# Optimization experiments

Hardware: AMD Instinct MI355X
Metric: run time of the kernel (lower is better)

Reference implementation:

```python
import jax, jax.numpy as jnp
import numpy as np

B = 16384        # batch size
K = 50           # neighbors per user (fixed for static shapes)
T = B * K        # total gathered neighbor items
NNEG = 20        # negative samples per positive
D = 128          # embedding dim
N_USERS = 100000
N_ITEMS = 100000
ALPHA = 1.0


def setup_inputs() -> dict:
    key = jax.random.key(0)
    k = jax.random.split(key, 9)
    I = jax.random.randint(k[0], (B,), 0, N_ITEMS)
    U = jax.random.randint(k[1], (B,), 0, N_USERS)
    I_neg = jax.random.randint(k[2], (B, NNEG), 0, N_ITEMS)
    I_U = jax.random.randint(k[3], (T,), 0, N_ITEMS)
    N_U = jnp.full((B,), K, dtype=jnp.int32)
    I_in_I_U = jax.random.randint(k[4], (B,), 0, 2).astype(jnp.int32)
    P_emb = jax.random.normal(k[5], (N_ITEMS, D), jnp.float32) * 0.02
    Q_emb = jax.random.normal(k[6], (N_ITEMS, D), jnp.float32) * 0.02
    b_u = jax.random.normal(k[7], (N_USERS,), jnp.float32) * 0.01
    b_i = jax.random.normal(k[8], (N_ITEMS,), jnp.float32) * 0.01
    return {"I": I, "U": U, "I_neg": I_neg, "I_U": I_U, "N_U": N_U,
            "I_in_I_U": I_in_I_U, "P_emb": P_emb, "Q_emb": Q_emb,
            "b_u": b_u, "b_i": b_i}


def reference(I, U, I_neg, I_U, N_U, I_in_I_U, P_emb, Q_emb, b_u, b_i):
    # P(.) / Q(.) abstracted as embedding lookups
    q = Q_emb[I]                     # [B, D]
    p = P_emb[I_U]                   # [T, D]
    p_self = P_emb[I]                # [B, D]

    # scatter-add neighbor embeddings into per-row sums
    U_idx = jnp.repeat(jnp.arange(B), N_U, total_repeat_length=T)  # [T]
    p_sum = jax.ops.segment_sum(p, U_idx, num_segments=B)          # [B, D]

    ind = I_in_I_U.astype(q.dtype)                                 # [B]
    p_ctx = p_sum - p_self * ind[:, None]                          # exclude self
    div = jnp.clip(N_U.astype(q.dtype) - ind, 1.0, None) ** ALPHA  # [B]
    p_ctx_avg = p_ctx / div[:, None]

    pq = jnp.sum(p_ctx_avg * q, axis=1)                            # [B]
    r = b_u[U] + b_i[I] + pq

    q_neg = Q_emb[I_neg.reshape(-1)].reshape(B, NNEG, D)
    pq_neg = jnp.einsum('bd,bnd->bn', p_ctx_avg, q_neg)            # [B, NNEG]
    r_neg = b_u[U][:, None] + b_i[I_neg] + pq_neg
    return (r, r_neg)
```

## Files before the change

### kernel.cpp

```cpp
#include <hip/hip_runtime.h>


constexpr int B_SZ    = 16384;
constexpr int K_NB    = 50;
constexpr int NNEG    = 20;
constexpr int D_DIM   = 128;
constexpr int N_ITEMS = 100000;

constexpr size_t TBL_ELEMS = (size_t)N_ITEMS * D_DIM;
constexpr size_t OFF_P   = 0;
constexpr size_t OFF_Q   = TBL_ELEMS;
constexpr size_t WS_NEED = 2 * TBL_ELEMS;

__device__ __forceinline__ uint32_t enc_e4m3(float x) {
    x = fminf(fmaxf(x, -448.f), 448.f);
    uint32_t b = __float_as_uint(x * 0x1p-120f);
    uint32_t s = b >> 31;
    uint32_t m = b & 0x7fffffffu;
    m = m + 0x7ffffu + ((m >> 20) & 1u);
    return (s << 7) | ((m >> 20) & 0x7fu);
}

#ifndef HW_FP8
#if defined(__has_builtin)
#if __has_builtin(__builtin_amdgcn_cvt_pk_f32_fp8)
#define HW_FP8 1
#endif
#endif
#endif
#ifndef HW_FP8
#define HW_FP8 0
#endif

typedef float f32x2_t __attribute__((ext_vector_type(2)));

__device__ __forceinline__ void dec_fp8x4(uint32_t w, float* f) {
#if HW_FP8
    f32x2_t lo = __builtin_amdgcn_cvt_pk_f32_fp8((int)w, false);
    f32x2_t hi = __builtin_amdgcn_cvt_pk_f32_fp8((int)w, true);
    f[0] = lo[0]; f[1] = lo[1]; f[2] = hi[0]; f[3] = hi[1];
#else
    #pragma unroll
    for (int j = 0; j < 4; ++j) {
        const uint32_t b = w >> (8 * j);
        const uint32_t bits = ((b & 0x80u) << 24) | ((b & 0x7fu) << 20);
        f[j] = __uint_as_float(bits) * 0x1p120f;
    }
#endif
}
__device__ __forceinline__ void dec_fp8x8(uint2 v, float* f) {
    dec_fp8x4(v.x, f);
    dec_fp8x4(v.y, f + 4);
}

__global__ __launch_bounds__(256) void cvt_tables(
    const float4* __restrict__ P4, const float4* __restrict__ Q4,
    unsigned char* __restrict__ ws, int p_thr)
{
    int i = blockIdx.x * blockDim.x + threadIdx.x;
    const float4* src; uint32_t* dst;
    if (i < p_thr) { src = P4; dst = (uint32_t*)(ws + OFF_P); }
    else           { src = Q4; dst = (uint32_t*)(ws + OFF_Q); i -= p_thr; }
    const float4 v = src[i];
    const uint32_t o = enc_e4m3(v.x * 64.f)
                     | (enc_e4m3(v.y * 64.f) << 8)
                     | (enc_e4m3(v.z * 64.f) << 16)
                     | (enc_e4m3(v.w * 64.f) << 24);
    dst[i] = o;
}

__global__ __launch_bounds__(256, 4) void fism_fwd_f8(
    const int* __restrict__ I,
    const int* __restrict__ U,
    const int* __restrict__ I_neg,
    const int* __restrict__ I_U,
    const int* __restrict__ N_U,
    const int* __restrict__ I_in_I_U,
    const unsigned char* __restrict__ ws,
    const float* __restrict__ b_u,
    const float* __restrict__ b_i,
    float* __restrict__ r,
    float* __restrict__ r_neg)
{
    const int wave = (blockIdx.x * blockDim.x + threadIdx.x) >> 6;
    if (wave >= B_SZ) return;
    const int lane = threadIdx.x & 63;
    const int t    = lane & 15;
    const int g    = lane >> 4;
    const int b    = wave;

    const unsigned char* Pb = ws + OFF_P;
    const unsigned char* Qb = ws + OFF_Q;

    int my_nbr = 0, my_neg = 0;
    if (lane < K_NB) my_nbr = I_U[b * K_NB + lane];
    if (lane < NNEG) my_neg = I_neg[b * NNEG + lane];
    const int   ii  = I[b];
    const int   uu  = U[b];
    const float ind = (float)I_in_I_U[b];
    const float nuf = (float)N_U[b];

    const float bu     = b_u[uu];
    const float bi_pos = b_i[ii];
    float my_bneg = 0.f;
    if (lane < NNEG) my_bneg = b_i[my_neg];

    const uint2 psu = *(const uint2*)(Pb + (size_t)ii * 128 + 8 * t);
    const uint2 qpu = *(const uint2*)(Qb + (size_t)ii * 128 + 8 * t);

    uint2 v[12];
    #pragma unroll
    for (int k = 0; k < 12; ++k) {
        const int item = __shfl(my_nbr, 4 * k + g, 64);
        v[k] = *(const uint2*)(Pb + (size_t)item * 128 + 8 * t);
    }
    const int item_t = __shfl(my_nbr, 48 + (g & 1), 64);
    uint2 vt = make_uint2(0u, 0u);
    if (g < 2) vt = *(const uint2*)(Pb + (size_t)item_t * 128 + 8 * t);

    uint2 qv[5];
    float bn[5];
    #pragma unroll
    for (int s = 0; s < 5; ++s) {
        const int n = 4 * s + g;
        const int item = __shfl(my_neg, n, 64);
        bn[s] = __shfl(my_bneg, n, 64);
        qv[s] = *(const uint2*)(Qb + (size_t)item * 128 + 8 * t);
    }

    float acc[8] = {0.f, 0.f, 0.f, 0.f, 0.f, 0.f, 0.f, 0.f};
    #pragma unroll
    for (int k = 0; k < 12; ++k) {
        float f[8]; dec_fp8x8(v[k], f);
        #pragma unroll
        for (int j = 0; j < 8; ++j) acc[j] += f[j];
    }
    {
        float f[8]; dec_fp8x8(vt, f);
        #pragma unroll
        for (int j = 0; j < 8; ++j) acc[j] += f[j];
    }
    #pragma unroll
    for (int j = 0; j < 8; ++j) {
        acc[j] += __shfl_xor(acc[j], 16, 64);
        acc[j] += __shfl_xor(acc[j], 32, 64);
    }

    float ps[8]; dec_fp8x8(psu, ps);
    const float inv = (1.0f / 4096.0f) / fmaxf(nuf - ind, 1.0f);
    float pctx[8];
    #pragma unroll
    for (int j = 0; j < 8; ++j) pctx[j] = (acc[j] - ps[j] * ind) * inv;

    {
        float qp[8]; dec_fp8x8(qpu, qp);
        float dot = 0.f;
        #pragma unroll
        for (int j = 0; j < 8; ++j) dot += pctx[j] * qp[j];
        #pragma unroll
        for (int m = 8; m > 0; m >>= 1)
            dot += __shfl_xor(dot, m, 64);
        if (lane == 0) r[b] = bu + bi_pos + dot;
    }

    #pragma unroll
    for (int s = 0; s < 5; ++s) {
        float q8[8]; dec_fp8x8(qv[s], q8);
        float d = 0.f;
        #pragma unroll
        for (int j = 0; j < 8; ++j) d += pctx[j] * q8[j];
        #pragma unroll
        for (int m = 8; m > 0; m >>= 1)
            d += __shfl_xor(d, m, 64);
        if (t == 0) r_neg[b * NNEG + 4 * s + g] = bu + bn[s] + d;
    }
}

__global__ __launch_bounds__(256) void fism_fwd(
    const int* __restrict__ I,
    const int* __restrict__ U,
    const int* __restrict__ I_neg,
    const int* __restrict__ I_U,
    const int* __restrict__ N_U,
    const int* __restrict__ I_in_I_U,
    const float* __restrict__ P,
    const float* __restrict__ Q,
    const float* __restrict__ b_u,
    const float* __restrict__ b_i,
    float* __restrict__ r,
    float* __restrict__ r_neg)
{
    const int wave = (blockIdx.x * blockDim.x + threadIdx.x) >> 6;
    if (wave >= B_SZ) return;
    const int lane = threadIdx.x & 63;
    const int sl   = lane & 31;
    const int half = lane >> 5;
    const int b    = wave;

    int my_nbr = 0, my_neg = 0;
    if (lane < K_NB)  my_nbr = I_U[b * K_NB + lane];
    if (lane < NNEG)  my_neg = I_neg[b * NNEG + lane];
    const int   ii   = I[b];
    const int   uu   = U[b];
    const float ind  = (float)I_in_I_U[b];
    const float nuf  = (float)N_U[b];

    const float bu     = b_u[uu];
    const float bi_pos = b_i[ii];
    float my_bneg = 0.f;
    if (lane < NNEG) my_bneg = b_i[my_neg];

    const float4 ps = ((const float4*)(P + (size_t)ii * D_DIM))[sl];
    const float4 qp = ((const float4*)(Q + (size_t)ii * D_DIM))[sl];

    float4 acc = {0.f, 0.f, 0.f, 0.f};
    #pragma unroll 5
    for (int k = 0; k < K_NB / 2; ++k) {
        const int item = __shfl(my_nbr, 2 * k + half, 64);
        const float4 v = ((const float4*)(P + (size_t)item * D_DIM))[sl];
        acc.x += v.x; acc.y += v.y; acc.z += v.z; acc.w += v.w;
    }
    acc.x += __shfl_xor(acc.x, 32, 64);
    acc.y += __shfl_xor(acc.y, 32, 64);
    acc.z += __shfl_xor(acc.z, 32, 64);
    acc.w += __shfl_xor(acc.w, 32, 64);

    const float inv = 1.0f / fmaxf(nuf - ind, 1.0f);
    float4 pctx;
    pctx.x = (acc.x - ps.x * ind) * inv;
    pctx.y = (acc.y - ps.y * ind) * inv;
    pctx.z = (acc.z - ps.z * ind) * inv;
    pctx.w = (acc.w - ps.w * ind) * inv;

    {
        float dot = pctx.x * qp.x + pctx.y * qp.y + pctx.z * qp.z + pctx.w * qp.w;
        #pragma unroll
        for (int m = 16; m > 0; m >>= 1)
            dot += __shfl_xor(dot, m, 64);
        if (lane == 0) r[b] = bu + bi_pos + dot;
    }

    #pragma unroll 5
    for (int tN = 0; tN < NNEG / 2; ++tN) {
        const int   n    = 2 * tN + half;
        const int   item = __shfl(my_neg,  n, 64);
        const float bnv  = __shfl(my_bneg, n, 64);
        const float4 qv  = ((const float4*)(Q + (size_t)item * D_DIM))[sl];
        float d = pctx.x * qv.x + pctx.y * qv.y + pctx.z * qv.z + pctx.w * qv.w;
        #pragma unroll
        for (int m = 16; m > 0; m >>= 1)
            d += __shfl_xor(d, m, 64);
        if (sl == 0) r_neg[b * NNEG + n] = bu + bnv + d;
    }
}

extern "C" void kernel_launch(void* const* d_in, const int* in_sizes, int n_in,
                              void* d_out, int out_size, void* d_ws, size_t ws_size,
                              hipStream_t stream) {
    const int*   I        = (const int*)d_in[0];
    const int*   U        = (const int*)d_in[1];
    const int*   I_neg    = (const int*)d_in[2];
    const int*   I_U      = (const int*)d_in[3];
    const int*   N_U      = (const int*)d_in[4];
    const int*   I_in_I_U = (const int*)d_in[5];
    const float* P_emb    = (const float*)d_in[6];
    const float* Q_emb    = (const float*)d_in[7];
    const float* b_u      = (const float*)d_in[8];
    const float* b_i      = (const float*)d_in[9];

    float* r     = (float*)d_out;
    float* r_neg = (float*)d_out + B_SZ;

    if (d_ws && ws_size >= WS_NEED) {
        unsigned char* ws = (unsigned char*)d_ws;

        const int p_thr = (int)(TBL_ELEMS / 4);
        const int total = 2 * p_thr;
        cvt_tables<<<total / 256, 256, 0, stream>>>(
            (const float4*)P_emb, (const float4*)Q_emb, ws, p_thr);

        fism_fwd_f8<<<B_SZ / 4, 256, 0, stream>>>(
            I, U, I_neg, I_U, N_U, I_in_I_U, ws, b_u, b_i, r, r_neg);
    } else {
        fism_fwd<<<B_SZ / 4, 256, 0, stream>>>(
            I, U, I_neg, I_U, N_U, I_in_I_U, P_emb, Q_emb, b_u, b_i, r, r_neg);
    }
}
```

Before: 162.9 us.

## Quantize P table to int4 with per-row scales and widen lane tiling

Replaces the FP8 copy of the P embedding table with a 4-bit symmetric quantization that stores one scale per row. This halves the bytes gathered for the 50 neighbour rows. The Q table stays FP8, and lanes are regrouped into 8 groups of 8 lanes, each handling 16 elements, so every wave gathers more rows per load step. The cost is much coarser precision for P (15 levels per row), which may break tolerance. Both the conversion pass and the gather kernel change structure.

```diff
diff --git a/kernel.cpp b/kernel.cpp
--- a/kernel.cpp
+++ b/kernel.cpp
@@ -8,9 +8,10 @@
 constexpr int N_ITEMS = 100000;
 
 constexpr size_t TBL_ELEMS = (size_t)N_ITEMS * D_DIM;
-constexpr size_t OFF_P   = 0;
-constexpr size_t OFF_Q   = TBL_ELEMS;
-constexpr size_t WS_NEED = 2 * TBL_ELEMS;
+constexpr size_t OFF_P4 = 0;
+constexpr size_t OFF_SC = (size_t)N_ITEMS * 64;
+constexpr size_t OFF_Q  = OFF_SC + (size_t)N_ITEMS * 4;
+constexpr size_t WS_NEED = OFF_Q + TBL_ELEMS;
 
 __device__ __forceinline__ uint32_t enc_e4m3(float x) {
     x = fminf(fmaxf(x, -448.f), 448.f);
@@ -48,28 +49,74 @@
     }
 #endif
 }
-__device__ __forceinline__ void dec_fp8x8(uint2 v, float* f) {
+__device__ __forceinline__ void dec_fp8x16(uint4 v, float* f) {
     dec_fp8x4(v.x, f);
     dec_fp8x4(v.y, f + 4);
-}
-
+    dec_fp8x4(v.z, f + 8);
+    dec_fp8x4(v.w, f + 12);
+}
+
+__device__ __forceinline__ void acc_i4x16(uint2 w, float sc, float* acc) {
+    #pragma unroll
+    for (int j = 0; j < 8; ++j) {
+        const int n0 = (int)((w.x >> (4 * j)) & 15u);
+        const int n1 = (int)((w.y >> (4 * j)) & 15u);
+        acc[j]     = fmaf((float)((n0 ^ 8) - 8), sc, acc[j]);
+        acc[8 + j] = fmaf((float)((n1 ^ 8) - 8), sc, acc[8 + j]);
+    }
+}
+__device__ __forceinline__ void dec_i4x16(uint2 w, float sc, float* f) {
+    #pragma unroll
+    for (int j = 0; j < 8; ++j) {
+        const int n0 = (int)((w.x >> (4 * j)) & 15u);
+        const int n1 = (int)((w.y >> (4 * j)) & 15u);
+        f[j]     = (float)((n0 ^ 8) - 8) * sc;
+        f[8 + j] = (float)((n1 ^ 8) - 8) * sc;
+    }
+}
+
+constexpr int CVT_PBLK = 6250;
+constexpr int CVT_QBLK = 12500;
 __global__ __launch_bounds__(256) void cvt_tables(
     const float4* __restrict__ P4, const float4* __restrict__ Q4,
-    unsigned char* __restrict__ ws, int p_thr)
+    unsigned char* __restrict__ ws)
 {
-    int i = blockIdx.x * blockDim.x + threadIdx.x;
-    const float4* src; uint32_t* dst;
-    if (i < p_thr) { src = P4; dst = (uint32_t*)(ws + OFF_P); }
-    else           { src = Q4; dst = (uint32_t*)(ws + OFF_Q); i -= p_thr; }
-    const float4 v = src[i];
-    const uint32_t o = enc_e4m3(v.x * 64.f)
-                     | (enc_e4m3(v.y * 64.f) << 8)
-                     | (enc_e4m3(v.z * 64.f) << 16)
-                     | (enc_e4m3(v.w * 64.f) << 24);
-    dst[i] = o;
-}
-
-__global__ __launch_bounds__(256, 4) void fism_fwd_f8(
+    if (blockIdx.x < CVT_PBLK) {
+        const int w    = (blockIdx.x * 256 + threadIdx.x) >> 6;
+        const int lane = threadIdx.x & 63;
+        const int c    = lane & 15;
+        const int row  = w * 4 + (lane >> 4);
+        const float4 a = P4[(size_t)row * 32 + 2 * c];
+        const float4 d = P4[(size_t)row * 32 + 2 * c + 1];
+        float f[8] = {a.x, a.y, a.z, a.w, d.x, d.y, d.z, d.w};
+        float m = 0.f;
+        #pragma unroll
+        for (int j = 0; j < 8; ++j) m = fmaxf(m, fabsf(f[j]));
+        #pragma unroll
+        for (int s = 1; s < 16; s <<= 1) m = fmaxf(m, __shfl_xor(m, s, 64));
+        const float delta = (m > 0.f) ? m * (1.f / 7.f) : 1.f;
+        const float invd  = (m > 0.f) ? 7.f / m : 0.f;
+        uint32_t o = 0;
+        #pragma unroll
+        for (int j = 0; j < 8; ++j) {
+            int q = (int)rintf(f[j] * invd);
+            q = max(-7, min(7, q));
+            o |= ((uint32_t)(q & 0xF)) << (4 * j);
+        }
+        ((uint32_t*)(ws + OFF_P4))[(size_t)row * 16 + c] = o;
+        if (c == 0) ((float*)(ws + OFF_SC))[row] = delta;
+    } else {
+        const int i = (blockIdx.x - CVT_PBLK) * 256 + threadIdx.x;
+        const float4 v = Q4[i];
+        const uint32_t o = enc_e4m3(v.x * 64.f)
+                         | (enc_e4m3(v.y * 64.f) << 8)
+                         | (enc_e4m3(v.z * 64.f) << 16)
+                         | (enc_e4m3(v.w * 64.f) << 24);
+        ((uint32_t*)(ws + OFF_Q))[i] = o;
+    }
+}
+
+__global__ __launch_bounds__(256, 4) void fism_fwd_i4(
     const int* __restrict__ I,
     const int* __restrict__ U,
     const int* __restrict__ I_neg,
@@ -85,11 +132,12 @@
     const int wave = (blockIdx.x * blockDim.x + threadIdx.x) >> 6;
     if (wave >= B_SZ) return;
     const int lane = threadIdx.x & 63;
-    const int t    = lane & 15;
-    const int g    = lane >> 4;
+    const int o    = lane & 7;
+    const int gg   = lane >> 3;
     const int b    = wave;
 
-    const unsigned char* Pb = ws + OFF_P;
+    const unsigned char* Pb = ws + OFF_P4;
+    const float*         Sc = (const float*)(ws + OFF_SC);
     const unsigned char* Qb = ws + OFF_Q;
 
     int my_nbr = 0, my_neg = 0;
@@ -105,74 +153,77 @@
     float my_bneg = 0.f;
     if (lane < NNEG) my_bneg = b_i[my_neg];
 
-    const uint2 psu = *(const uint2*)(Pb + (size_t)ii * 128 + 8 * t);
-    const uint2 qpu = *(const uint2*)(Qb + (size_t)ii * 128 + 8 * t);
-
-    uint2 v[12];
-    #pragma unroll
-    for (int k = 0; k < 12; ++k) {
-        const int item = __shfl(my_nbr, 4 * k + g, 64);
-        v[k] = *(const uint2*)(Pb + (size_t)item * 128 + 8 * t);
-    }
-    const int item_t = __shfl(my_nbr, 48 + (g & 1), 64);
+    const uint2 psu   = *(const uint2*)(Pb + (size_t)ii * 64 + 8 * o);
+    const float sc_ii = Sc[ii];
+    const uint4 qpu   = *(const uint4*)(Qb + (size_t)ii * 128 + 16 * o);
+
+    uint2 v[6]; float scv[6];
+    #pragma unroll
+    for (int k = 0; k < 6; ++k) {
+        const int item = __shfl(my_nbr, 8 * k + gg, 64);
+        v[k]   = *(const uint2*)(Pb + (size_t)item * 64 + 8 * o);
+        scv[k] = Sc[item];
+    }
+    const int item_t = __shfl(my_nbr, 48 + (gg & 1), 64);
     uint2 vt = make_uint2(0u, 0u);
-    if (g < 2) vt = *(const uint2*)(Pb + (size_t)item_t * 128 + 8 * t);
-
-    uint2 qv[5];
-    float bn[5];
-    #pragma unroll
-    for (int s = 0; s < 5; ++s) {
-        const int n = 4 * s + g;
-        const int item = __shfl(my_neg, n, 64);
-        bn[s] = __shfl(my_bneg, n, 64);
-        qv[s] = *(const uint2*)(Qb + (size_t)item * 128 + 8 * t);
-    }
-
-    float acc[8] = {0.f, 0.f, 0.f, 0.f, 0.f, 0.f, 0.f, 0.f};
-    #pragma unroll
-    for (int k = 0; k < 12; ++k) {
-        float f[8]; dec_fp8x8(v[k], f);
-        #pragma unroll
-        for (int j = 0; j < 8; ++j) acc[j] += f[j];
-    }
-    {
-        float f[8]; dec_fp8x8(vt, f);
-        #pragma unroll
-        for (int j = 0; j < 8; ++j) acc[j] += f[j];
-    }
-    #pragma unroll
-    for (int j = 0; j < 8; ++j) {
+    float st = 0.f;
+    if (gg < 2) { vt = *(const uint2*)(Pb + (size_t)item_t * 64 + 8 * o);
+                  st = Sc[item_t]; }
+
+    uint4 qv[3]; float bn3[3];
+    #pragma unroll
+    for (int s = 0; s < 3; ++s) {
+        const int n  = 8 * s + gg;
+        const int nn = (n < NNEG) ? n : 0;
+        const int item = __shfl(my_neg, nn, 64);
+        bn3[s] = __shfl(my_bneg, nn, 64);
+        qv[s] = make_uint4(0u, 0u, 0u, 0u);
+        if (n < NNEG) qv[s] = *(const uint4*)(Qb + (size_t)item * 128 + 16 * o);
+    }
+
+    float acc[16];
+    #pragma unroll
+    for (int j = 0; j < 16; ++j) acc[j] = 0.f;
+    #pragma unroll
+    for (int k = 0; k < 6; ++k) acc_i4x16(v[k], scv[k], acc);
+    acc_i4x16(vt, st, acc);
+    #pragma unroll
+    for (int j = 0; j < 16; ++j) {
+        acc[j] += __shfl_xor(acc[j], 8, 64);
         acc[j] += __shfl_xor(acc[j], 16, 64);
         acc[j] += __shfl_xor(acc[j], 32, 64);
     }
 
-    float ps[8]; dec_fp8x8(psu, ps);
-    const float inv = (1.0f / 4096.0f) / fmaxf(nuf - ind, 1.0f);
-    float pctx[8];
-    #pragma unroll
-    for (int j = 0; j < 8; ++j) pctx[j] = (acc[j] - ps[j] * ind) * inv;
+    float ps[16]; dec_i4x16(psu, sc_ii, ps);
+    const float inv = (1.0f / 64.0f) / fmaxf(nuf - ind, 1.0f);
+    float pctx[16];
+    #pragma unroll
+    for (int j = 0; j < 16; ++j) pctx[j] = (acc[j] - ps[j] * ind) * inv;
 
     {
-        float qp[8]; dec_fp8x8(qpu, qp);
+        float qp[16]; dec_fp8x16(qpu, qp);
         float dot = 0.f;
         #pragma unroll
-        for (int j = 0; j < 8; ++j) dot += pctx[j] * qp[j];
-        #pragma unroll
-        for (int m = 8; m > 0; m >>= 1)
-            dot += __shfl_xor(dot, m, 64);
+        for (int j = 0; j < 16; ++j) dot += pctx[j] * qp[j];
+        dot += __shfl_xor(dot, 1, 64);
+        dot += __shfl_xor(dot, 2, 64);
+        dot += __shfl_xor(dot, 4, 64);
         if (lane == 0) r[b] = bu + bi_pos + dot;
     }
 
     #pragma unroll
-    for (int s = 0; s < 5; ++s) {
-        float q8[8]; dec_fp8x8(qv[s], q8);
-        float d = 0.f;
-        #pragma unroll
-        for (int j = 0; j < 8; ++j) d += pctx[j] * q8[j];
-        #pragma unroll
-        for (int m = 8; m > 0; m >>= 1)
-            d += __shfl_xor(d, m, 64);
-        if (t == 0) r_neg[b * NNEG + 4 * s + g] = bu + bn[s] + d;
+    for (int s = 0; s < 3; ++s) {
+        const int n = 8 * s + gg;
+        if (n < NNEG) {
+            float q16[16]; dec_fp8x16(qv[s], q16);
+            float d = 0.f;
+            #pragma unroll
+            for (int j = 0; j < 16; ++j) d += pctx[j] * q16[j];
+            d += __shfl_xor(d, 1, 64);
+            d += __shfl_xor(d, 2, 64);
+            d += __shfl_xor(d, 4, 64);
+            if (o == 0) r_neg[b * NNEG + n] = bu + bn3[s] + d;
+        }
     }
 }
 
@@ -274,12 +325,10 @@
     if (d_ws && ws_size >= WS_NEED) {
         unsigned char* ws = (unsigned char*)d_ws;
 
-        const int p_thr = (int)(TBL_ELEMS / 4);
-        const int total = 2 * p_thr;
-        cvt_tables<<<total / 256, 256, 0, stream>>>(
-            (const float4*)P_emb, (const float4*)Q_emb, ws, p_thr);
-
-        fism_fwd_f8<<<B_SZ / 4, 256, 0, stream>>>(
+        cvt_tables<<<CVT_PBLK + CVT_QBLK, 256, 0, stream>>>(
+            (const float4*)P_emb, (const float4*)Q_emb, ws);
+
+        fism_fwd_i4<<<B_SZ / 4, 256, 0, stream>>>(
             I, U, I_neg, I_U, N_U, I_in_I_U, ws, b_u, b_i, r, r_neg);
     } else {
         fism_fwd<<<B_SZ / 4, 256, 0, stream>>>(
```

Result: no change. 163.7 us (+0.5%).
